# Kernel optimization log

Hardware: AMD Instinct MI355X
Metric: run time of the kernel (lower is better)

## Reference

```python
import jax, jax.numpy as jnp
import numpy as np

N_NODES = 50000
IN_NF = 64
HID = 128
OUT_NF = 64
EDGE_HID = HID // 2  # edge_nf_ratio = 2
N_LAYERS = 4
N_EDGES = 800000
NUM_LATENT_NODES = 64
C_EVEN = 1.0
C_ODD = 2.0 / NUM_LATENT_NODES


def setup_inputs() -> dict:
    key = jax.random.key(0)
    ks = jax.random.split(key, 24)
    def lin(k, fan_in, fan_out):
        # torch nn.Linear default init: U(-1/sqrt(fan_in), 1/sqrt(fan_in))
        bound = 1.0 / np.sqrt(fan_in)
        kw, kb = jax.random.split(k)
        w = jax.random.uniform(kw, (fan_in, fan_out), jnp.float32, -bound, bound)
        b = jax.random.uniform(kb, (fan_out,), jnp.float32, -bound, bound)
        return w, b

    h = jax.random.normal(ks[0], (N_NODES, IN_NF), jnp.float32)
    edges_a = jax.random.randint(ks[1], (2, N_EDGES), 0, N_NODES, jnp.int32)
    edges_b = jax.random.randint(ks[2], (2, N_EDGES), 0, N_NODES, jnp.int32)
    update_mask_a = jax.random.randint(ks[3], (N_NODES, 1), 0, 2, jnp.int32).astype(bool)
    update_mask_b = jax.random.randint(ks[4], (N_NODES, 1), 0, 2, jnp.int32).astype(bool)

    emb_in_w, emb_in_b = lin(ks[5], IN_NF, HID)
    emb_out_w, emb_out_b = lin(ks[6], HID, OUT_NF)

    ew1, eb1, ew2, eb2 = [], [], [], []
    nw1, nb1, nw2, nb2 = [], [], [], []
    for i in range(N_LAYERS):
        w, b = lin(ks[7 + i], 2 * HID, EDGE_HID); ew1.append(w); eb1.append(b)
        w, b = lin(ks[11 + i], EDGE_HID, EDGE_HID); ew2.append(w); eb2.append(b)
        w, b = lin(ks[15 + i], HID + EDGE_HID, HID); nw1.append(w); nb1.append(b)
        w, b = lin(ks[19 + i], HID, HID); nw2.append(w); nb2.append(b)

    stack = lambda xs: jnp.stack(xs, 0)
    return {
        "h": h, "edges_a": edges_a, "edges_b": edges_b,
        "update_mask_a": update_mask_a, "update_mask_b": update_mask_b,
        "emb_in_w": emb_in_w, "emb_in_b": emb_in_b,
        "emb_out_w": emb_out_w, "emb_out_b": emb_out_b,
        "edge_w1": stack(ew1), "edge_b1": stack(eb1),
        "edge_w2": stack(ew2), "edge_b2": stack(eb2),
        "node_w1": stack(nw1), "node_b1": stack(nb1),
        "node_w2": stack(nw2), "node_b2": stack(nb2),
    }


def _gcl(h, edges, mask, C, ew1, eb1, ew2, eb2, nw1, nb1, nw2, nb2):
    row, col = edges[0], edges[1]
    # edge model: gather source/target node feats -> 2-layer SiLU MLP
    feat = jnp.concatenate([h[row], h[col]], axis=-1)      # [E, 2*HID]
    m = jax.nn.silu(feat @ ew1 + eb1)                      # [E, EDGE_HID]
    m = jax.nn.silu(m @ ew2 + eb2)                         # [E, EDGE_HID]
    # aggregate messages to receiving nodes (scatter-add), scaled by C
    agg = jax.ops.segment_sum(m, row, num_segments=h.shape[0]) * C
    # node model with residual
    upd = jax.nn.silu(jnp.concatenate([h, agg], axis=-1) @ nw1 + nb1) @ nw2 + nb2
    h_new = h + upd
    # masked asynchronous update: only nodes with mask=True are updated
    return jnp.where(mask, h_new, h)


def reference(h, edges_a, edges_b, update_mask_a, update_mask_b,
              emb_in_w, emb_in_b, emb_out_w, emb_out_b,
              edge_w1, edge_b1, edge_w2, edge_b2,
              node_w1, node_b1, node_w2, node_b2):
    h = h @ emb_in_w + emb_in_b
    for i in range(N_LAYERS):
        if i % 2 == 0:
            edges, mask, C = edges_a, update_mask_a, C_EVEN
        else:
            edges, mask, C = edges_b, update_mask_b, C_ODD
        h = _gcl(h, edges, mask, C,
                 edge_w1[i], edge_b1[i], edge_w2[i], edge_b2[i],
                 node_w1[i], node_b1[i], node_w2[i], node_b2[i])
    h = h @ emb_out_w + emb_out_b
    return h
```

## Files before the change

### kernel.cpp

```cpp
#include <hip/hip_runtime.h>
#include <cstdint>

typedef __bf16 bf16_t;
typedef bf16_t bf16x8 __attribute__((ext_vector_type(8)));
typedef float floatx4 __attribute__((ext_vector_type(4)));
typedef unsigned short ushort4v __attribute__((ext_vector_type(4)));

constexpr int N_NODES = 50000;
constexpr int N_EDGES = 800000;
constexpr int HID = 128;
constexpr int EH = 64;
constexpr int NCH = (N_NODES + 255) / 256;

__device__ __forceinline__ float silu_f(float x) {
    return x * __builtin_amdgcn_rcpf(1.0f + __expf(-x));
}

__global__ __launch_bounds__(256) void pack_all_kernel(
    const float* __restrict__ embin, const float* __restrict__ embout,
    const float* __restrict__ ew1, const float* __restrict__ ew2,
    const float* __restrict__ nw1, const float* __restrict__ nw2,
    bf16_t* __restrict__ pk)
{
    int t = blockIdx.x * 256 + threadIdx.x;
    if (t >= 32768) {
        t -= 32768;
        int lane = t & 63, chunk = t >> 6;
        int ks = chunk & 3, nt = (chunk >> 2) & 7, l = chunk >> 5;
        int quad = lane >> 4, coln = lane & 15;
        const float* Wl = ew1 + l * 256 * 64;
        int kb = (nt >= 4 ? 128 : 0) + ks * 32 + quad * 8;
        int nc = (nt & 3) * 16 + coln;
        bf16x8 v;
#pragma unroll
        for (int j = 0; j < 8; j++) v[j] = (bf16_t)Wl[(kb + j) * 64 + nc];
        *(bf16x8*)(pk + 262144 + t * 8) = v;
        return;
    }
    const float* W; int K, Nc; int base; bf16_t* out;
    if (t < 1024)       { W = embin;  K = 64;  Nc = 128; base = 0;     out = pk; }
    else if (t < 2048)  { W = embout; K = 128; Nc = 64;  base = 1024;  out = pk + 8192; }
    else if (t < 10240) { W = ew1;    K = 256; Nc = 64;  base = 2048;  out = pk + 16384; }
    else if (t < 12288) { W = ew2;    K = 64;  Nc = 64;  base = 10240; out = pk + 81920; }
    else if (t < 24576) { W = nw1;    K = 192; Nc = 128; base = 12288; out = pk + 98304; }
    else                { W = nw2;    K = 128; Nc = 128; base = 24576; out = pk + 196608; }
    t -= base;
    int KS = K >> 5, NT = Nc >> 4;
    int lane = t & 63;
    int chunk = t >> 6;
    int ks = chunk % KS;
    int nt = (chunk / KS) % NT;
    int l  = chunk / (KS * NT);
    int quad = lane >> 4, coln = lane & 15;
    const float* Wl = W + l * K * Nc;
    bf16x8 v;
#pragma unroll
    for (int j = 0; j < 8; j++)
        v[j] = (bf16_t)Wl[(ks * 32 + quad * 8 + j) * Nc + nt * 16 + coln];
    *(bf16x8*)(out + t * 8) = v;
}

__global__ void hist2_kernel(const int* __restrict__ ea, const int* __restrict__ eb,
                             const int* __restrict__ ma, const int* __restrict__ mb,
                             int* __restrict__ ba, int* __restrict__ bb) {
    int half = gridDim.x >> 1;
    int b = blockIdx.x;
    const int* erows; const int* mask; int* bins;
    if (b < half) { erows = ea; mask = ma; bins = ba; }
    else          { erows = eb; mask = mb; bins = bb; b -= half; }
    int i = b * 256 + threadIdx.x;
    if (i >= N_EDGES) return;
    int r = erows[i];
    if (mask[r] != 0) atomicAdd(&bins[r], 1);
}

__global__ __launch_bounds__(256) void scan_phase1(
    const int* __restrict__ bins_a, const int* __restrict__ bins_b,
    int* __restrict__ bs_a, int* __restrict__ bs_b) {
    const int* bins = blockIdx.y ? bins_b : bins_a;
    int* bs = blockIdx.y ? bs_b : bs_a;
    int i = blockIdx.x * 256 + threadIdx.x;
    int v = (i < N_NODES) ? (bins[i] != 0 ? bins[i] : 0) : 0;
#pragma unroll
    for (int off = 32; off; off >>= 1) v += __shfl_down(v, off, 64);
    __shared__ int ws_[4];
    int lane = threadIdx.x & 63, wv = threadIdx.x >> 6;
    if (lane == 0) ws_[wv] = v;
    __syncthreads();
    if (threadIdx.x == 0) bs[blockIdx.x] = ws_[0] + ws_[1] + ws_[2] + ws_[3];
}

__global__ __launch_bounds__(256) void scan_phase2(
    int* __restrict__ bs_a, int* __restrict__ bs_b,
    int* __restrict__ bins_a, int* __restrict__ bins_b) {
    int* bs = blockIdx.x ? bs_b : bs_a;
    int* bins = blockIdx.x ? bins_b : bins_a;
    int t = threadIdx.x, lane = t & 63, wv = t >> 6;
    int v = (t < NCH) ? bs[t] : 0;
    int s = v;
#pragma unroll
    for (int off = 1; off < 64; off <<= 1) {
        int u = __shfl_up(s, off, 64);
        if (lane >= off) s += u;
    }
    __shared__ int wsum[4];
    if (lane == 63) wsum[wv] = s;
    __syncthreads();
    int woff = 0;
    for (int w = 0; w < wv; w++) woff += wsum[w];
    int excl = s - v + woff;
    if (t < NCH) bs[t] = excl;
    if (t == NCH - 1) bins[N_NODES] = excl + v;
}

__global__ __launch_bounds__(256) void mask_scan2(
    int* __restrict__ ms_a, int* __restrict__ ms_b,
    int* __restrict__ cnt_a, int* __restrict__ cnt_b) {
    int* ms = blockIdx.x ? ms_b : ms_a;
    int* cnt = blockIdx.x ? cnt_b : cnt_a;
    int t = threadIdx.x, lane = t & 63, wv = t >> 6;
    int v = (t < NCH) ? ms[t] : 0;
    int s = v;
#pragma unroll
    for (int off = 1; off < 64; off <<= 1) {
        int u = __shfl_up(s, off, 64);
        if (lane >= off) s += u;
    }
    __shared__ int wsum[4];
    if (lane == 63) wsum[wv] = s;
    __syncthreads();
    int woff = 0;
    for (int w = 0; w < wv; w++) woff += wsum[w];
    int excl = s - v + woff;
    if (t < NCH) ms[t] = excl;
    if (t == NCH - 1) cnt[0] = excl + v;
}

__global__ __launch_bounds__(256) void compact_kernel(
    const int* __restrict__ ma, const int* __restrict__ mb,
    const int* __restrict__ ms_a, const int* __restrict__ ms_b,
    int* __restrict__ la, int* __restrict__ lb) {
    const int* mask = blockIdx.y ? mb : ma;
    const int* ms = blockIdx.y ? ms_b : ms_a;
    int* list = blockIdx.y ? lb : la;
    int i = blockIdx.x * 256 + threadIdx.x;
    int t = threadIdx.x, lane = t & 63, wv = t >> 6;
    int m = (i < N_NODES) ? (mask[i] != 0) : 0;
    unsigned long long bal = __ballot(m != 0);
    int pos = (int)__popcll(bal & ((1ull << lane) - 1ull));
    __shared__ int wsum[4];
    if (lane == 63) wsum[wv] = pos + m;
    __syncthreads();
    int woff = 0;
    for (int w = 0; w < wv; w++) woff += wsum[w];
    if (m) list[ms[blockIdx.x] + woff + pos] = i;
}

__global__ __launch_bounds__(256) void scan_phase3(
    int* __restrict__ bins_a, int* __restrict__ bins_b,
    const int* __restrict__ bs_a, const int* __restrict__ bs_b) {
    int* bins = blockIdx.y ? bins_b : bins_a;
    const int* bs = blockIdx.y ? bs_b : bs_a;
    int i = blockIdx.x * 256 + threadIdx.x;
    int t = threadIdx.x, lane = t & 63, wv = t >> 6;
    int v = (i < N_NODES) ? bins[i] : 0;
    int s = v;
#pragma unroll
    for (int off = 1; off < 64; off <<= 1) {
        int u = __shfl_up(s, off, 64);
        if (lane >= off) s += u;
    }
    __shared__ int wsum[4];
    if (lane == 63) wsum[wv] = s;
    __syncthreads();
    int woff = 0;
    for (int w = 0; w < wv; w++) woff += wsum[w];
    if (i < N_NODES) bins[i] = s - v + woff + bs[blockIdx.x];
}

__global__ void fill_src_kernel(const int* __restrict__ bins_a, const int* __restrict__ bins_b,
                                int* __restrict__ ssrc_a, int* __restrict__ ssrc_b) {
    const int* bins = blockIdx.y ? bins_b : bins_a;
    int* ssrc = blockIdx.y ? ssrc_b : ssrc_a;
    int r = blockIdx.x * 256 + threadIdx.x;
    if (r >= N_NODES) return;
    int p0 = bins[r], p1 = bins[r + 1];
    for (int p = p0; p < p1; p++) ssrc[p] = r;
}

__global__ void scatter2_kernel(const int* __restrict__ ea, const int* __restrict__ eb,
                                const int* __restrict__ ma, const int* __restrict__ mb,
                                int* __restrict__ ba, int* __restrict__ bb,
                                int* __restrict__ sdst_a, int* __restrict__ sdst_b) {
    int half = gridDim.x >> 1;
    int b = blockIdx.x;
    const int* e; const int* mask; int* bins; int* sdst;
    if (b < half) { e = ea; mask = ma; bins = ba; sdst = sdst_a; }
    else          { e = eb; mask = mb; bins = bb; sdst = sdst_b; b -= half; }
    int i = b * 256 + threadIdx.x;
    if (i >= N_EDGES) return;
    int r = e[i];
    if (mask[r] == 0) return;
    int c = e[N_EDGES + i];
    int pos = atomicAdd(&bins[r], 1);
    sdst[pos] = c;
}

__global__ __launch_bounds__(256) void emb_in_kernel(
    const float* __restrict__ h0, const bf16_t* __restrict__ wp,
    const float* __restrict__ bias, float* __restrict__ h, bf16_t* __restrict__ h_bf)
{
    int t = threadIdx.x, wave = t >> 6, lane = t & 63;
    int quad = lane >> 4, col = lane & 15;
    int m0 = blockIdx.x * 64 + wave * 16;
    int ndc = min(m0 + col, N_NODES - 1);
    floatx4 acc[8] = {};
#pragma unroll
    for (int ks = 0; ks < 2; ks++) {
        const float* ap = h0 + ndc * 64 + ks * 32 + quad * 8;
        floatx4 f0 = *(const floatx4*)ap;
        floatx4 f1 = *(const floatx4*)(ap + 4);
        bf16x8 a;
#pragma unroll
        for (int j = 0; j < 4; j++) { a[j] = (bf16_t)f0[j]; a[j + 4] = (bf16_t)f1[j]; }
#pragma unroll
        for (int nt = 0; nt < 8; nt++) {
            bf16x8 b = ((const bf16x8*)wp)[(nt * 2 + ks) * 64 + lane];
            acc[nt] = __builtin_amdgcn_mfma_f32_16x16x32_bf16(a, b, acc[nt], 0, 0, 0);
        }
    }
#pragma unroll
    for (int r = 0; r < 4; r++) {
        int nd2 = m0 + quad * 4 + r;
        if (nd2 < N_NODES) {
#pragma unroll
            for (int nt = 0; nt < 8; nt++) {
                int n = nt * 16 + col;
                float x = acc[nt][r] + bias[n];
                h[nd2 * HID + n] = x;
                h_bf[nd2 * HID + n] = (bf16_t)x;
            }
        }
    }
}

__global__ __launch_bounds__(256) void pre_edge_kernel(
    const bf16_t* __restrict__ h_bf, const bf16_t* __restrict__ w1cat,
    const float* __restrict__ b1, float* __restrict__ P)
{
    int t = threadIdx.x, wave = t >> 6, lane = t & 63;
    int quad = lane >> 4, col = lane & 15;
    int m0 = blockIdx.x * 64 + wave * 16;
    int ndc = min(m0 + col, N_NODES - 1);
    floatx4 acc[8] = {};
#pragma unroll
    for (int ks = 0; ks < 4; ks++) {
        bf16x8 a = *(const bf16x8*)(h_bf + ndc * HID + ks * 32 + quad * 8);
#pragma unroll
        for (int nt = 0; nt < 8; nt++) {
            bf16x8 b = ((const bf16x8*)w1cat)[(nt * 4 + ks) * 64 + lane];
            acc[nt] = __builtin_amdgcn_mfma_f32_16x16x32_bf16(a, b, acc[nt], 0, 0, 0);
        }
    }
#pragma unroll
    for (int r = 0; r < 4; r++) {
        int nd2 = m0 + quad * 4 + r;
        if (nd2 < N_NODES) {
#pragma unroll
            for (int nt = 0; nt < 8; nt++) {
                int n = nt * 16 + col;
                float x = acc[nt][r] + (nt >= 4 ? b1[n - 64] : 0.0f);
                P[nd2 * 128 + n] = x;
            }
        }
    }
}

__global__ __launch_bounds__(256, 4) void edge_kernel_pre(
    const float* __restrict__ P, const int* __restrict__ ssrc,
    const int* __restrict__ sdst, const int* __restrict__ m_ptr,
    const bf16_t* __restrict__ w2p, const float* __restrict__ b2,
    float* __restrict__ agg, float C)
{
    __shared__ __align__(16) bf16_t pool[4][64 * 40];

    int t = threadIdx.x;
    int wave = t >> 6, lane = t & 63, quad = lane >> 4, col = lane & 15;
    bf16_t* mbT = pool[wave];

    float b2v[4];
#pragma unroll
    for (int nt = 0; nt < 4; nt++) b2v[nt] = b2[nt * 16 + col];

    int M = m_ptr[0];
    int ntiles = (M + 31) >> 5;
    int wid = blockIdx.x * 4 + wave, nw = gridDim.x * 4;
    if (wid >= ntiles) return;

    int sr = 0x7fffffff, ds = 0x7fffffff;
    { int p = wid * 32 + lane; if (lane < 32 && p < M) { sr = ssrc[p]; ds = sdst[p]; } }

    for (int tile = wid; tile < ntiles; tile += nw) {
        int tnc = min(tile + nw, ntiles - 1);
        int srn = 0x7fffffff, dsn = 0x7fffffff;
        { int p = tnc * 32 + lane; if (lane < 32 && p < M) { srn = ssrc[p]; dsn = sdst[p]; } }

        floatx4 acc2[2][4] = {};
#pragma unroll
        for (int m = 0; m < 2; m++) {
            int rN = min(__shfl(sr, m * 16 + col, 64), N_NODES - 1);
            int cN = min(__shfl(ds, m * 16 + col, 64), N_NODES - 1);
            const float* pr = P + rN * 128 + quad * 8;
            const float* pc = P + cN * 128 + 64 + quad * 8;
            floatx4 fr[4], fc[4];
#pragma unroll
            for (int ks = 0; ks < 2; ks++) {
                fr[ks * 2]     = *(const floatx4*)(pr + ks * 32);
                fr[ks * 2 + 1] = *(const floatx4*)(pr + ks * 32 + 4);
                fc[ks * 2]     = *(const floatx4*)(pc + ks * 32);
                fc[ks * 2 + 1] = *(const floatx4*)(pc + ks * 32 + 4);
            }
#pragma unroll
            for (int ks = 0; ks < 2; ks++) {
                bf16x8 a2;
#pragma unroll
                for (int j = 0; j < 4; j++) {
                    a2[j]     = (bf16_t)silu_f(fr[ks * 2][j]     + fc[ks * 2][j]);
                    a2[j + 4] = (bf16_t)silu_f(fr[ks * 2 + 1][j] + fc[ks * 2 + 1][j]);
                }
#pragma unroll
                for (int nt = 0; nt < 4; nt++) {
                    bf16x8 b = ((const bf16x8*)w2p)[(nt * 2 + ks) * 64 + lane];
                    acc2[m][nt] = __builtin_amdgcn_mfma_f32_16x16x32_bf16(a2, b, acc2[m][nt], 0, 0, 0);
                }
            }
        }

#pragma unroll
        for (int m = 0; m < 2; m++)
#pragma unroll
            for (int nt = 0; nt < 4; nt++) {
                ushort4v pv;
#pragma unroll
                for (int r = 0; r < 4; r++) {
                    bf16_t bv = (bf16_t)(silu_f(acc2[m][nt][r] + b2v[nt]) * C);
                    pv[r] = __builtin_bit_cast(unsigned short, bv);
                }
                *(ushort4v*)(mbT + (nt * 16 + col) * 40 + m * 16 + quad * 4) = pv;
            }

        {
            float mv[32];
#pragma unroll
            for (int i = 0; i < 4; i++) {
                bf16x8 v8 = *(const bf16x8*)(mbT + lane * 40 + i * 8);
#pragma unroll
                for (int j = 0; j < 8; j++) mv[i * 8 + j] = (float)v8[j];
            }
            int dp = __shfl(sr, 0, 64);
            float run = mv[0];
#pragma unroll
            for (int r = 1; r < 32; r++) {
                int d = __shfl(sr, r, 64);
                if (d != dp) {
                    if (dp < N_NODES) atomicAdd(agg + dp * EH + lane, run);
                    run = mv[r]; dp = d;
                } else run += mv[r];
            }
            if (dp < N_NODES) atomicAdd(agg + dp * EH + lane, run);
        }

        sr = srn; ds = dsn;
    }
}

__global__ __launch_bounds__(256, 3) void edge_kernel_sorted(
    const bf16_t* __restrict__ h_bf, const int* __restrict__ ssrc,
    const int* __restrict__ sdst, const int* __restrict__ m_ptr,
    const bf16_t* __restrict__ w1p, const float* __restrict__ b1,
    const bf16_t* __restrict__ w2p, const float* __restrict__ b2,
    float* __restrict__ agg, float C)
{
    __shared__ __align__(16) bf16_t w1s[16384];
    __shared__ __align__(16) bf16_t pool[4][64 * 40];

    int t = threadIdx.x;
#pragma unroll
    for (int i = 0; i < 8; i++)
        ((bf16x8*)w1s)[t + 256 * i] = ((const bf16x8*)w1p)[t + 256 * i];
    __syncthreads();

    int wave = t >> 6, lane = t & 63, quad = lane >> 4, col = lane & 15;
    bf16_t* hl = pool[wave];
    bf16_t* mbT = pool[wave];

    float b1v[4], b2v[4];
#pragma unroll
    for (int nt = 0; nt < 4; nt++) { b1v[nt] = b1[nt * 16 + col]; b2v[nt] = b2[nt * 16 + col]; }

    int M = m_ptr[0];
    int ntiles = (M + 31) >> 5;
    int wid = blockIdx.x * 4 + wave, nw = gridDim.x * 4;
    if (wid >= ntiles) return;

    int sr = 0x7fffffff, ds = 0x7fffffff;
    { int p = wid * 32 + lane; if (lane < 32 && p < M) { sr = ssrc[p]; ds = sdst[p]; } }
    bf16x8 a[2][8];
    {
        int ns0 = min(__shfl(sr, col, 64), N_NODES - 1);
        int ns1 = min(__shfl(sr, 16 + col, 64), N_NODES - 1);
        int nd0 = min(__shfl(ds, col, 64), N_NODES - 1);
        int nd1 = min(__shfl(ds, 16 + col, 64), N_NODES - 1);
#pragma unroll
        for (int ks = 0; ks < 8; ks++) {
            int o = (ks & 3) * 32 + quad * 8;
            a[0][ks] = *(const bf16x8*)(h_bf + (ks < 4 ? ns0 : nd0) * HID + o);
            a[1][ks] = *(const bf16x8*)(h_bf + (ks < 4 ? ns1 : nd1) * HID + o);
        }
    }

    for (int tile = wid; tile < ntiles; tile += nw) {
        int tnc = min(tile + nw, ntiles - 1);
        int srn = 0x7fffffff, dsn = 0x7fffffff;
        { int p = tnc * 32 + lane; if (lane < 32 && p < M) { srn = ssrc[p]; dsn = sdst[p]; } }

        floatx4 acc[2][4] = {};
#pragma unroll
        for (int ks = 0; ks < 8; ks++) {
#pragma unroll
            for (int nt = 0; nt < 4; nt++) {
                bf16x8 b = ((const bf16x8*)w1s)[(nt * 8 + ks) * 64 + lane];
                acc[0][nt] = __builtin_amdgcn_mfma_f32_16x16x32_bf16(a[0][ks], b, acc[0][nt], 0, 0, 0);
                acc[1][nt] = __builtin_amdgcn_mfma_f32_16x16x32_bf16(a[1][ks], b, acc[1][nt], 0, 0, 0);
            }
        }

        bf16x8 an[2][8];
        {
            int ns0 = min(__shfl(srn, col, 64), N_NODES - 1);
            int ns1 = min(__shfl(srn, 16 + col, 64), N_NODES - 1);
            int nd0 = min(__shfl(dsn, col, 64), N_NODES - 1);
            int nd1 = min(__shfl(dsn, 16 + col, 64), N_NODES - 1);
#pragma unroll
            for (int ks = 0; ks < 8; ks++) {
                int o = (ks & 3) * 32 + quad * 8;
                an[0][ks] = *(const bf16x8*)(h_bf + (ks < 4 ? ns0 : nd0) * HID + o);
                an[1][ks] = *(const bf16x8*)(h_bf + (ks < 4 ? ns1 : nd1) * HID + o);
            }
        }

#pragma unroll
        for (int m = 0; m < 2; m++)
#pragma unroll
            for (int nt = 0; nt < 4; nt++)
#pragma unroll
                for (int r = 0; r < 4; r++)
                    hl[(m * 16 + quad * 4 + r) * 72 + nt * 16 + col] =
                        (bf16_t)silu_f(acc[m][nt][r] + b1v[nt]);

        floatx4 acc2[2][4] = {};
#pragma unroll
        for (int ks = 0; ks < 2; ks++) {
            bf16x8 a2[2];
#pragma unroll
            for (int m = 0; m < 2; m++)
                a2[m] = *(const bf16x8*)(hl + (m * 16 + col) * 72 + ks * 32 + quad * 8);
#pragma unroll
            for (int nt = 0; nt < 4; nt++) {
                bf16x8 b = ((const bf16x8*)w2p)[(nt * 2 + ks) * 64 + lane];
                acc2[0][nt] = __builtin_amdgcn_mfma_f32_16x16x32_bf16(a2[0], b, acc2[0][nt], 0, 0, 0);
                acc2[1][nt] = __builtin_amdgcn_mfma_f32_16x16x32_bf16(a2[1], b, acc2[1][nt], 0, 0, 0);
            }
        }
#pragma unroll
        for (int m = 0; m < 2; m++)
#pragma unroll
            for (int nt = 0; nt < 4; nt++) {
                ushort4v p;
#pragma unroll
                for (int r = 0; r < 4; r++) {
                    bf16_t bv = (bf16_t)(silu_f(acc2[m][nt][r] + b2v[nt]) * C);
                    p[r] = __builtin_bit_cast(unsigned short, bv);
                }
                *(ushort4v*)(mbT + (nt * 16 + col) * 40 + m * 16 + quad * 4) = p;
            }

        {
            float mv[32];
#pragma unroll
            for (int i = 0; i < 4; i++) {
                bf16x8 v8 = *(const bf16x8*)(mbT + lane * 40 + i * 8);
#pragma unroll
                for (int j = 0; j < 8; j++) mv[i * 8 + j] = (float)v8[j];
            }
            int dp = __shfl(sr, 0, 64);
            float run = mv[0];
#pragma unroll
            for (int r = 1; r < 32; r++) {
                int d = __shfl(sr, r, 64);
                if (d != dp) {
                    if (dp < N_NODES) atomicAdd(agg + dp * EH + lane, run);
                    run = mv[r]; dp = d;
                } else run += mv[r];
            }
            if (dp < N_NODES) atomicAdd(agg + dp * EH + lane, run);
        }

        sr = srn; ds = dsn;
#pragma unroll
        for (int m = 0; m < 2; m++)
#pragma unroll
            for (int ks = 0; ks < 8; ks++) a[m][ks] = an[m][ks];
    }
}

__global__ __launch_bounds__(256) void edge_kernel(
    const bf16_t* __restrict__ h_bf, const int* __restrict__ edges,
    const int* __restrict__ mask,
    const bf16_t* __restrict__ w1p, const float* __restrict__ b1,
    const bf16_t* __restrict__ w2p, const float* __restrict__ b2,
    float* __restrict__ agg, float C)
{
    __shared__ __align__(16) bf16_t w1s[16384];
    __shared__ __align__(16) bf16_t w2s[4096];
    __shared__ __align__(16) bf16_t hl[4][16 * 72];

    int t = threadIdx.x;
#pragma unroll
    for (int i = 0; i < 8; i++)
        ((bf16x8*)w1s)[t + 256 * i] = ((const bf16x8*)w1p)[t + 256 * i];
#pragma unroll
    for (int i = 0; i < 2; i++)
        ((bf16x8*)w2s)[t + 256 * i] = ((const bf16x8*)w2p)[t + 256 * i];
    __syncthreads();

    int wave = t >> 6, lane = t & 63, quad = lane >> 4, col = lane & 15;
    bf16_t* myhl = hl[wave];

    float b1v[4], b2v[4];
#pragma unroll
    for (int nt = 0; nt < 4; nt++) { b1v[nt] = b1[nt * 16 + col]; b2v[nt] = b2[nt * 16 + col]; }

    const int ntile_cnt = N_EDGES / 64;
    for (int tile = blockIdx.x; tile < ntile_cnt; tile += gridDim.x) {
        int ebase = tile * 64 + wave * 16;
        int src = edges[ebase + col];
        int dst = edges[N_EDGES + ebase + col];

        floatx4 acc[4] = {};
#pragma unroll
        for (int ks = 0; ks < 8; ks++) {
            int idx = (ks < 4) ? src : dst;
            bf16x8 a = *(const bf16x8*)(h_bf + idx * HID + (ks & 3) * 32 + quad * 8);
#pragma unroll
            for (int nt = 0; nt < 4; nt++) {
                bf16x8 b = ((const bf16x8*)w1s)[(nt * 8 + ks) * 64 + lane];
                acc[nt] = __builtin_amdgcn_mfma_f32_16x16x32_bf16(a, b, acc[nt], 0, 0, 0);
            }
        }
#pragma unroll
        for (int nt = 0; nt < 4; nt++)
#pragma unroll
            for (int r = 0; r < 4; r++)
                myhl[(quad * 4 + r) * 72 + nt * 16 + col] = (bf16_t)silu_f(acc[nt][r] + b1v[nt]);
        __syncthreads();

        floatx4 acc2[4] = {};
#pragma unroll
        for (int ks = 0; ks < 2; ks++) {
            bf16x8 a = *(const bf16x8*)(myhl + col * 72 + ks * 32 + quad * 8);
#pragma unroll
            for (int nt = 0; nt < 4; nt++) {
                bf16x8 b = ((const bf16x8*)w2s)[(nt * 2 + ks) * 64 + lane];
                acc2[nt] = __builtin_amdgcn_mfma_f32_16x16x32_bf16(a, b, acc2[nt], 0, 0, 0);
            }
        }
#pragma unroll
        for (int r = 0; r < 4; r++) {
            int dest = edges[ebase + quad * 4 + r];
            if (mask[dest] != 0) {
                float* aggp = agg + dest * EH;
#pragma unroll
                for (int nt = 0; nt < 4; nt++) {
                    float x = acc2[nt][r] + b2v[nt];
                    atomicAdd(aggp + nt * 16 + col, silu_f(x) * C);
                }
            }
        }
        __syncthreads();
    }
}

__global__ __launch_bounds__(256) void node_kernel_masked(
    float* __restrict__ h, bf16_t* __restrict__ h_bf,
    float* __restrict__ agg, const int* __restrict__ list,
// ... 111 lines not shown
            myhl[(quad * 4 + r) * 136 + nt * 16 + col] = (bf16_t)silu_f(x);
        }

    floatx4 acc2[8] = {};
#pragma unroll
    for (int ks = 0; ks < 4; ks++) {
        bf16x8 a = *(const bf16x8*)(myhl + col * 136 + ks * 32 + quad * 8);
#pragma unroll
        for (int nt = 0; nt < 8; nt++) {
            bf16x8 b = ((const bf16x8*)w2p)[(nt * 4 + ks) * 64 + lane];
            acc2[nt] = __builtin_amdgcn_mfma_f32_16x16x32_bf16(a, b, acc2[nt], 0, 0, 0);
        }
    }
#pragma unroll
    for (int r = 0; r < 4; r++) {
        int nd2 = m0 + quad * 4 + r;
        bool valid = nd2 < N_NODES;
        bool upd = valid && mask[min(nd2, N_NODES - 1)] != 0;
        if (upd) {
#pragma unroll
            for (int nt = 0; nt < 8; nt++) {
                int n = nt * 16 + col;
                float hv = h[nd2 * HID + n] + acc2[nt][r] + b2[n];
                h[nd2 * HID + n] = hv;
                bf16_t hb = (bf16_t)hv;
                h_bf[nd2 * HID + n] = hb;
                myhl[(quad * 4 + r) * 136 + n] = hb;
            }
        } else {
#pragma unroll
            for (int nt = 0; nt < 8; nt++) {
                int n = nt * 16 + col;
                myhl[(quad * 4 + r) * 136 + n] =
                    valid ? h_bf[nd2 * HID + n] : (bf16_t)0.0f;
            }
        }
    }
    floatx4 ao[4] = {};
#pragma unroll
    for (int ks = 0; ks < 4; ks++) {
        bf16x8 a = *(const bf16x8*)(myhl + col * 136 + ks * 32 + quad * 8);
#pragma unroll
        for (int nt = 0; nt < 4; nt++) {
            bf16x8 b = ((const bf16x8*)wop)[(nt * 4 + ks) * 64 + lane];
            ao[nt] = __builtin_amdgcn_mfma_f32_16x16x32_bf16(a, b, ao[nt], 0, 0, 0);
        }
    }
#pragma unroll
    for (int r = 0; r < 4; r++) {
        int nd2 = m0 + quad * 4 + r;
        if (nd2 < N_NODES) {
#pragma unroll
            for (int nt = 0; nt < 4; nt++) {
                int n = nt * 16 + col;
                out[nd2 * 64 + n] = ao[nt][r] + bo[n];
            }
        }
    }
}

extern "C" void kernel_launch(void* const* d_in, const int* in_sizes, int n_in,
                              void* d_out, int out_size, void* d_ws, size_t ws_size,
                              hipStream_t stream) {
    const float* h0        = (const float*)d_in[0];
    const int*   edges_a   = (const int*)d_in[1];
    const int*   edges_b   = (const int*)d_in[2];
    const int*   mask_a    = (const int*)d_in[3];
    const int*   mask_b    = (const int*)d_in[4];
    const float* emb_in_w  = (const float*)d_in[5];
    const float* emb_in_b  = (const float*)d_in[6];
    const float* emb_out_w = (const float*)d_in[7];
    const float* emb_out_b = (const float*)d_in[8];
    const float* ew1 = (const float*)d_in[9];
    const float* eb1 = (const float*)d_in[10];
    const float* ew2 = (const float*)d_in[11];
    const float* eb2 = (const float*)d_in[12];
    const float* nw1 = (const float*)d_in[13];
    const float* nb1 = (const float*)d_in[14];
    const float* nw2 = (const float*)d_in[15];
    const float* nb2 = (const float*)d_in[16];

    const size_t SZ_H = 25600000, SZ_HBF = 12800000, SZ_AGG = 12800000;
    const size_t SZ_PK = 655360;
    const size_t SZ_S = 3200000, SZ_BINS = 200704, SZ_BS = 1024, SZ_LIST = 200704;
    const size_t SZ_P = 25600000;

    char* ws = (char*)d_ws;
    size_t off = 0;
    float*  h    = (float*)(ws + off);  off += SZ_H;
    bf16_t* h_bf = (bf16_t*)(ws + off); off += SZ_HBF;
    float*  agg  = (float*)(ws + off);  off += SZ_AGG;
    bf16_t* pk   = (bf16_t*)(ws + off); off += SZ_PK;
    int* ssrc_a = (int*)(ws + off); off += SZ_S;
    int* sdst_a = (int*)(ws + off); off += SZ_S;
    int* ssrc_b = (int*)(ws + off); off += SZ_S;
    int* sdst_b = (int*)(ws + off); off += SZ_S;
    int* bins_a = (int*)(ws + off); off += SZ_BINS;
    int* bins_b = (int*)(ws + off); off += SZ_BINS;
    int* bs_a   = (int*)(ws + off); off += SZ_BS;
    int* bs_b   = (int*)(ws + off); off += SZ_BS;
    int* ms_a   = (int*)(ws + off); off += SZ_BS;
    int* ms_b   = (int*)(ws + off); off += SZ_BS;
    int* cnt_a  = (int*)(ws + off); off += 256;
    int* cnt_b  = (int*)(ws + off); off += 256;
    int* list_a = (int*)(ws + off); off += SZ_LIST;
    int* list_b = (int*)(ws + off); off += SZ_LIST;
    bool sorted_path = (ws_size >= off);
    float* P = (float*)(ws + off); off += SZ_P;
    bool pre_path = (ws_size >= off);

    bf16_t* pk_embin  = pk;
    bf16_t* pk_embout = pk + 8192;
    bf16_t* pk_ew1    = pk + 16384;
    bf16_t* pk_ew2    = pk + 81920;
    bf16_t* pk_nw1    = pk + 98304;
    bf16_t* pk_nw2    = pk + 196608;
    bf16_t* pk_ew1cat = pk + 262144;

    pack_all_kernel<<<160, 256, 0, stream>>>(emb_in_w, emb_out_w, ew1, ew2, nw1, nw2, pk);

    const int edge_grid = (N_EDGES + 255) / 256;
    const int node_blocks = (N_NODES + 63) / 64;
    if (sorted_path) {
        hipMemsetAsync(bins_a, 0, 2 * SZ_BINS + 2 * SZ_BS, stream);
        hist2_kernel<<<2 * edge_grid, 256, 0, stream>>>(edges_a, edges_b, mask_a, mask_b,
                                                        bins_a, bins_b);
        scan_phase1<<<dim3(NCH, 2), 256, 0, stream>>>(bins_a, bins_b, bs_a, bs_b);
        scan_phase2<<<2, 256, 0, stream>>>(bs_a, bs_b, bins_a, bins_b);
        scan_phase3<<<dim3(NCH, 2), 256, 0, stream>>>(bins_a, bins_b, bs_a, bs_b);
        fill_src_kernel<<<dim3(NCH, 2), 256, 0, stream>>>(bins_a, bins_b, ssrc_a, ssrc_b);
        scatter2_kernel<<<2 * edge_grid, 256, 0, stream>>>(edges_a, edges_b, mask_a, mask_b,
                                                           bins_a, bins_b, sdst_a, sdst_b);
        scan_phase1<<<dim3(NCH, 2), 256, 0, stream>>>(mask_a, mask_b, ms_a, ms_b);
        mask_scan2<<<2, 256, 0, stream>>>(ms_a, ms_b, cnt_a, cnt_b);
        compact_kernel<<<dim3(NCH, 2), 256, 0, stream>>>(mask_a, mask_b, ms_a, ms_b,
                                                         list_a, list_b);
    }

    hipMemsetAsync(agg, 0, (size_t)N_NODES * EH * 4, stream);
    emb_in_kernel<<<node_blocks, 256, 0, stream>>>(h0, pk_embin, emb_in_b, h, h_bf);

    for (int l = 0; l < 4; l++) {
        const int* mask = (l & 1) ? mask_b : mask_a;
        float C = (l & 1) ? 0.03125f : 1.0f;
        if (pre_path) {
            const int* ssrc = (l & 1) ? ssrc_b : ssrc_a;
            const int* sdst = (l & 1) ? sdst_b : sdst_a;
            const int* mp   = ((l & 1) ? bins_b : bins_a) + N_NODES;
            pre_edge_kernel<<<node_blocks, 256, 0, stream>>>(
                h_bf, pk_ew1cat + l * 16384, eb1 + l * 64, P);
            edge_kernel_pre<<<1024, 256, 0, stream>>>(P, ssrc, sdst, mp,
                                                      pk_ew2 + l * 4096, eb2 + l * 64,
                                                      agg, C);
        } else if (sorted_path) {
            const int* ssrc = (l & 1) ? ssrc_b : ssrc_a;
            const int* sdst = (l & 1) ? sdst_b : sdst_a;
            const int* mp   = ((l & 1) ? bins_b : bins_a) + N_NODES;
            edge_kernel_sorted<<<768, 256, 0, stream>>>(h_bf, ssrc, sdst, mp,
                                                        pk_ew1 + l * 16384, eb1 + l * 64,
                                                        pk_ew2 + l * 4096,  eb2 + l * 64,
                                                        agg, C);
        } else {
            const int* edges = (l & 1) ? edges_b : edges_a;
            edge_kernel<<<768, 256, 0, stream>>>(h_bf, edges, mask,
                                                 pk_ew1 + l * 16384, eb1 + l * 64,
                                                 pk_ew2 + l * 4096,  eb2 + l * 64,
                                                 agg, C);
        }
        if (l < 3 && sorted_path) {
            const int* list = (l & 1) ? list_b : list_a;
            const int* cnt  = (l & 1) ? cnt_b : cnt_a;
            node_kernel_masked<<<node_blocks, 256, 0, stream>>>(
                h, h_bf, agg, list, cnt,
                pk_nw1 + l * 24576, nb1 + l * 128,
                pk_nw2 + l * 16384, nb2 + l * 128);
        } else if (l < 3) {
            node_kernel<<<node_blocks, 256, 0, stream>>>(h, h_bf, agg, mask,
                                                         pk_nw1 + l * 24576, nb1 + l * 128,
                                                         pk_nw2 + l * 16384, nb2 + l * 128,
                                                         pk_embout, emb_out_b, (float*)d_out);
            hipMemsetAsync(agg, 0, (size_t)N_NODES * EH * 4, stream);
        } else {
            node_kernel<<<node_blocks, 256, 0, stream>>>(h, h_bf, agg, mask,
                                                         pk_nw1 + 3 * 24576, nb1 + 3 * 128,
                                                         pk_nw2 + 3 * 16384, nb2 + 3 * 128,
                                                         pk_embout, emb_out_b, (float*)d_out);
        }
    }
}
```

Baseline: 439.8 us.

## Replace CSR sort with two-level bucket sort and fuse first pre-edge into embedding

The per-node histogram/scan/fill/scatter pipeline that builds sorted edge lists is replaced by a two-level bucket sort: edges are binned into 256-node buckets with shared-memory counters, then each bucket is sorted locally. This cuts global atomics and the number of preprocessing kernel launches. The first layer's pre-edge projection is fused into the input-embedding kernel, and the agg memset is merged with the bucket-counter memset. Buckets are capped at a fixed capacity, so edges beyond it would be silently dropped if a bucket overflowed.

```diff
diff --git a/kernel.cpp b/kernel.cpp
--- a/kernel.cpp
+++ b/kernel.cpp
@@ -11,6 +11,7 @@
 constexpr int HID = 128;
 constexpr int EH = 64;
 constexpr int NCH = (N_NODES + 255) / 256;
+constexpr int BKT_CAP = 4096;
 
 __device__ __forceinline__ float silu_f(float x) {
     return x * __builtin_amdgcn_rcpf(1.0f + __expf(-x));
@@ -60,18 +61,125 @@
     *(bf16x8*)(out + t * 8) = v;
 }
 
-__global__ void hist2_kernel(const int* __restrict__ ea, const int* __restrict__ eb,
-                             const int* __restrict__ ma, const int* __restrict__ mb,
-                             int* __restrict__ ba, int* __restrict__ bb) {
-    int half = gridDim.x >> 1;
-    int b = blockIdx.x;
-    const int* erows; const int* mask; int* bins;
-    if (b < half) { erows = ea; mask = ma; bins = ba; }
-    else          { erows = eb; mask = mb; bins = bb; b -= half; }
-    int i = b * 256 + threadIdx.x;
-    if (i >= N_EDGES) return;
-    int r = erows[i];
-    if (mask[r] != 0) atomicAdd(&bins[r], 1);
+__global__ __launch_bounds__(256) void bucketize_kernel(
+    const int* __restrict__ ea, const int* __restrict__ eb,
+    const int* __restrict__ ma, const int* __restrict__ mb,
+    int* __restrict__ gcur, int* __restrict__ gbuf)
+{
+    int g = blockIdx.y;
+    const int* e    = g ? eb : ea;
+    const int* mask = g ? mb : ma;
+    int* cur = gcur + g * 256;
+    int* buf = gbuf + g * 256 * BKT_CAP;
+    __shared__ int cnt[256];
+    int t = threadIdx.x;
+    cnt[t] = 0;
+    __syncthreads();
+    int base = blockIdx.x * 2048;
+    int r[8], c[8]; bool v[8];
+#pragma unroll
+    for (int k = 0; k < 8; k++) {
+        int i = base + k * 256 + t;
+        bool ok = i < N_EDGES;
+        int ii = ok ? i : 0;
+        int rr = e[ii];
+        int cc = e[N_EDGES + ii];
+        v[k] = ok && (mask[rr] != 0);
+        r[k] = rr; c[k] = cc;
+        if (v[k]) atomicAdd(&cnt[rr >> 8], 1);
+    }
+    __syncthreads();
+    int lc = cnt[t];
+    int gb = 0;
+    if (lc > 0) gb = atomicAdd(&cur[t], lc);
+    cnt[t] = gb;
+    __syncthreads();
+#pragma unroll
+    for (int k = 0; k < 8; k++) {
+        if (v[k]) {
+            int bkt = r[k] >> 8;
+            int p = atomicAdd(&cnt[bkt], 1);
+            if (p < BKT_CAP)
+                buf[bkt * BKT_CAP + p] = ((r[k] & 255) << 16) | c[k];
+        }
+    }
+}
+
+__global__ __launch_bounds__(256) void bucket_scan_kernel(
+    const int* __restrict__ gcur, int* __restrict__ bases,
+    int* __restrict__ mcnt_a, int* __restrict__ mcnt_b)
+{
+    int g = blockIdx.x;
+    const int* cur = gcur + g * 256;
+    int t = threadIdx.x, lane = t & 63, wv = t >> 6;
+    int v = (t < NCH) ? min(cur[t], BKT_CAP) : 0;
+    int s = v;
+#pragma unroll
+    for (int off = 1; off < 64; off <<= 1) {
+        int u = __shfl_up(s, off, 64);
+        if (lane >= off) s += u;
+    }
+    __shared__ int wsum[4];
+    if (lane == 63) wsum[wv] = s;
+    __syncthreads();
+    int woff = 0;
+    for (int w = 0; w < wv; w++) woff += wsum[w];
+    int excl = s - v + woff;
+    bases[g * 256 + t] = excl;
+    if (t == NCH - 1) *(g ? mcnt_b : mcnt_a) = excl + v;
+}
+
+__global__ __launch_bounds__(256) void bucket_sort_kernel(
+    const int* __restrict__ gcur, const int* __restrict__ gbuf,
+    const int* __restrict__ bases,
+    int* __restrict__ ssrc_a, int* __restrict__ sdst_a,
+    int* __restrict__ ssrc_b, int* __restrict__ sdst_b)
+{
+    int g = blockIdx.y, b = blockIdx.x;
+    const int* buf = gbuf + g * 256 * BKT_CAP + b * BKT_CAP;
+    int* ssrc = g ? ssrc_b : ssrc_a;
+    int* sdst = g ? sdst_b : sdst_a;
+    int cnt_e = min(gcur[g * 256 + b], BKT_CAP);
+    int base = bases[g * 256 + b];
+    __shared__ int h[256];
+    __shared__ int wsum[4];
+    int t = threadIdx.x, lane = t & 63, wv = t >> 6;
+    h[t] = 0;
+    __syncthreads();
+    int vals[16]; bool vv[16];
+#pragma unroll
+    for (int k = 0; k < 16; k++) {
+        int j = k * 256 + t;
+        vv[k] = j < cnt_e;
+        int x = vv[k] ? buf[j] : 0;
+        vals[k] = x;
+        if (vv[k]) atomicAdd(&h[x >> 16], 1);
+    }
+    __syncthreads();
+    int v = h[t];
+    int s = v;
+#pragma unroll
+    for (int off = 1; off < 64; off <<= 1) {
+        int u = __shfl_up(s, off, 64);
+        if (lane >= off) s += u;
+    }
+    if (lane == 63) wsum[wv] = s;
+    __syncthreads();
+    int woff = 0;
+    for (int w = 0; w < wv; w++) woff += wsum[w];
+    h[t] = s - v + woff;
+    __syncthreads();
+#pragma unroll
+    for (int k = 0; k < 16; k++) {
+        if (vv[k]) {
+            int x = vals[k];
+            int rl = x >> 16, c = x & 0xFFFF;
+            int p = atomicAdd(&h[rl], 1);
+            int gp = base + p;
+            ssrc[gp] = (b << 8) + rl;
+            sdst[gp] = c;
+        }
+    }
 }
 
 __global__ __launch_bounds__(256) void scan_phase1(
@@ -88,29 +196,6 @@
     if (lane == 0) ws_[wv] = v;
     __syncthreads();
     if (threadIdx.x == 0) bs[blockIdx.x] = ws_[0] + ws_[1] + ws_[2] + ws_[3];
-}
-
-__global__ __launch_bounds__(256) void scan_phase2(
-    int* __restrict__ bs_a, int* __restrict__ bs_b,
-    int* __restrict__ bins_a, int* __restrict__ bins_b) {
-    int* bs = blockIdx.x ? bs_b : bs_a;
-    int* bins = blockIdx.x ? bins_b : bins_a;
-    int t = threadIdx.x, lane = t & 63, wv = t >> 6;
-    int v = (t < NCH) ? bs[t] : 0;
-    int s = v;
-#pragma unroll
-    for (int off = 1; off < 64; off <<= 1) {
-        int u = __shfl_up(s, off, 64);
-        if (lane >= off) s += u;
-    }
-    __shared__ int wsum[4];
-    if (lane == 63) wsum[wv] = s;
-    __syncthreads();
-    int woff = 0;
-    for (int w = 0; w < wv; w++) woff += wsum[w];
-    int excl = s - v + woff;
-    if (t < NCH) bs[t] = excl;
-    if (t == NCH - 1) bins[N_NODES] = excl + v;
 }
 
 __global__ __launch_bounds__(256) void mask_scan2(
@@ -156,56 +241,6 @@
     if (m) list[ms[blockIdx.x] + woff + pos] = i;
 }
 
-__global__ __launch_bounds__(256) void scan_phase3(
-    int* __restrict__ bins_a, int* __restrict__ bins_b,
-    const int* __restrict__ bs_a, const int* __restrict__ bs_b) {
-    int* bins = blockIdx.y ? bins_b : bins_a;
-    const int* bs = blockIdx.y ? bs_b : bs_a;
-    int i = blockIdx.x * 256 + threadIdx.x;
-    int t = threadIdx.x, lane = t & 63, wv = t >> 6;
-    int v = (i < N_NODES) ? bins[i] : 0;
-    int s = v;
-#pragma unroll
-    for (int off = 1; off < 64; off <<= 1) {
-        int u = __shfl_up(s, off, 64);
-        if (lane >= off) s += u;
-    }
-    __shared__ int wsum[4];
-    if (lane == 63) wsum[wv] = s;
-    __syncthreads();
-    int woff = 0;
-    for (int w = 0; w < wv; w++) woff += wsum[w];
-    if (i < N_NODES) bins[i] = s - v + woff + bs[blockIdx.x];
-}
-
-__global__ void fill_src_kernel(const int* __restrict__ bins_a, const int* __restrict__ bins_b,
-                                int* __restrict__ ssrc_a, int* __restrict__ ssrc_b) {
-    const int* bins = blockIdx.y ? bins_b : bins_a;
-    int* ssrc = blockIdx.y ? ssrc_b : ssrc_a;
-    int r = blockIdx.x * 256 + threadIdx.x;
-    if (r >= N_NODES) return;
-    int p0 = bins[r], p1 = bins[r + 1];
-    for (int p = p0; p < p1; p++) ssrc[p] = r;
-}
-
-__global__ void scatter2_kernel(const int* __restrict__ ea, const int* __restrict__ eb,
-                                const int* __restrict__ ma, const int* __restrict__ mb,
-                                int* __restrict__ ba, int* __restrict__ bb,
-                                int* __restrict__ sdst_a, int* __restrict__ sdst_b) {
-    int half = gridDim.x >> 1;
-    int b = blockIdx.x;
-    const int* e; const int* mask; int* bins; int* sdst;
-    if (b < half) { e = ea; mask = ma; bins = ba; sdst = sdst_a; }
-    else          { e = eb; mask = mb; bins = bb; sdst = sdst_b; b -= half; }
-    int i = b * 256 + threadIdx.x;
-    if (i >= N_EDGES) return;
-    int r = e[i];
-    if (mask[r] == 0) return;
-    int c = e[N_EDGES + i];
-    int pos = atomicAdd(&bins[r], 1);
-    sdst[pos] = c;
-}
-
 __global__ __launch_bounds__(256) void emb_in_kernel(
     const float* __restrict__ h0, const bf16_t* __restrict__ wp,
     const float* __restrict__ bias, float* __restrict__ h, bf16_t* __restrict__ h_bf)
@@ -239,6 +274,74 @@
                 float x = acc[nt][r] + bias[n];
                 h[nd2 * HID + n] = x;
                 h_bf[nd2 * HID + n] = (bf16_t)x;
+            }
+        }
+    }
+}
+
+__global__ __launch_bounds__(256) void emb_in_p0_kernel(
+    const float* __restrict__ h0, const bf16_t* __restrict__ wp,
+    const float* __restrict__ bias, float* __restrict__ h, bf16_t* __restrict__ h_bf,
+    const bf16_t* __restrict__ w1cat, const float* __restrict__ b1,
+    float* __restrict__ P)
+{
+    __shared__ __align__(16) bf16_t hl[4][16 * 136];
+    int t = threadIdx.x, wave = t >> 6, lane = t & 63;
+    int quad = lane >> 4, col = lane & 15;
+    int m0 = blockIdx.x * 64 + wave * 16;
+    int ndc = min(m0 + col, N_NODES - 1);
+    floatx4 acc[8] = {};
+#pragma unroll
+    for (int ks = 0; ks < 2; ks++) {
+        const float* ap = h0 + ndc * 64 + ks * 32 + quad * 8;
+        floatx4 f0 = *(const floatx4*)ap;
+        floatx4 f1 = *(const floatx4*)(ap + 4);
+        bf16x8 a;
+#pragma unroll
+        for (int j = 0; j < 4; j++) { a[j] = (bf16_t)f0[j]; a[j + 4] = (bf16_t)f1[j]; }
+#pragma unroll
+        for (int nt = 0; nt < 8; nt++) {
+            bf16x8 b = ((const bf16x8*)wp)[(nt * 2 + ks) * 64 + lane];
+            acc[nt] = __builtin_amdgcn_mfma_f32_16x16x32_bf16(a, b, acc[nt], 0, 0, 0);
+        }
+    }
+    bf16_t* myhl = hl[wave];
+#pragma unroll
+    for (int r = 0; r < 4; r++) {
+        int nd2 = m0 + quad * 4 + r;
+        bool valid = nd2 < N_NODES;
+#pragma unroll
+        for (int nt = 0; nt < 8; nt++) {
+            int n = nt * 16 + col;
+            if (valid) {
+                float x = acc[nt][r] + bias[n];
+                h[nd2 * HID + n] = x;
+                bf16_t hb = (bf16_t)x;
+                h_bf[nd2 * HID + n] = hb;
+                myhl[(quad * 4 + r) * 136 + n] = hb;
+            } else {
+                myhl[(quad * 4 + r) * 136 + n] = (bf16_t)0.0f;
+            }
+        }
+    }
+    floatx4 accp[8] = {};
+#pragma unroll
+    for (int ks = 0; ks < 4; ks++) {
+        bf16x8 a = *(const bf16x8*)(myhl + col * 136 + ks * 32 + quad * 8);
+#pragma unroll
+        for (int nt = 0; nt < 8; nt++) {
+            bf16x8 b = ((const bf16x8*)w1cat)[(nt * 4 + ks) * 64 + lane];
+            accp[nt] = __builtin_amdgcn_mfma_f32_16x16x32_bf16(a, b, accp[nt], 0, 0, 0);
+        }
+    }
+#pragma unroll
+    for (int r = 0; r < 4; r++) {
+        int nd2 = m0 + quad * 4 + r;
+        if (nd2 < N_NODES) {
+#pragma unroll
+            for (int nt = 0; nt < 8; nt++) {
+                int n = nt * 16 + col;
+                P[nd2 * 128 + n] = accp[nt][r] + (nt >= 4 ? b1[n - 64] : 0.0f);
             }
         }
     }
@@ -371,146 +474,6 @@
         }
 
         sr = srn; ds = dsn;
-    }
-}
-
-__global__ __launch_bounds__(256, 3) void edge_kernel_sorted(
-    const bf16_t* __restrict__ h_bf, const int* __restrict__ ssrc,
-    const int* __restrict__ sdst, const int* __restrict__ m_ptr,
-    const bf16_t* __restrict__ w1p, const float* __restrict__ b1,
-    const bf16_t* __restrict__ w2p, const float* __restrict__ b2,
-    float* __restrict__ agg, float C)
-{
-    __shared__ __align__(16) bf16_t w1s[16384];
-    __shared__ __align__(16) bf16_t pool[4][64 * 40];
-
-    int t = threadIdx.x;
-#pragma unroll
-    for (int i = 0; i < 8; i++)
-        ((bf16x8*)w1s)[t + 256 * i] = ((const bf16x8*)w1p)[t + 256 * i];
-    __syncthreads();
-
-    int wave = t >> 6, lane = t & 63, quad = lane >> 4, col = lane & 15;
-    bf16_t* hl = pool[wave];
-    bf16_t* mbT = pool[wave];
-
-    float b1v[4], b2v[4];
-#pragma unroll
-    for (int nt = 0; nt < 4; nt++) { b1v[nt] = b1[nt * 16 + col]; b2v[nt] = b2[nt * 16 + col]; }
-
-    int M = m_ptr[0];
-    int ntiles = (M + 31) >> 5;
-    int wid = blockIdx.x * 4 + wave, nw = gridDim.x * 4;
-    if (wid >= ntiles) return;
-
-    int sr = 0x7fffffff, ds = 0x7fffffff;
-    { int p = wid * 32 + lane; if (lane < 32 && p < M) { sr = ssrc[p]; ds = sdst[p]; } }
-    bf16x8 a[2][8];
-    {
-        int ns0 = min(__shfl(sr, col, 64), N_NODES - 1);
-        int ns1 = min(__shfl(sr, 16 + col, 64), N_NODES - 1);
-        int nd0 = min(__shfl(ds, col, 64), N_NODES - 1);
-        int nd1 = min(__shfl(ds, 16 + col, 64), N_NODES - 1);
-#pragma unroll
-        for (int ks = 0; ks < 8; ks++) {
-            int o = (ks & 3) * 32 + quad * 8;
-            a[0][ks] = *(const bf16x8*)(h_bf + (ks < 4 ? ns0 : nd0) * HID + o);
-            a[1][ks] = *(const bf16x8*)(h_bf + (ks < 4 ? ns1 : nd1) * HID + o);
-        }
-    }
-
-    for (int tile = wid; tile < ntiles; tile += nw) {
-        int tnc = min(tile + nw, ntiles - 1);
-        int srn = 0x7fffffff, dsn = 0x7fffffff;
-        { int p = tnc * 32 + lane; if (lane < 32 && p < M) { srn = ssrc[p]; dsn = sdst[p]; } }
-
-        floatx4 acc[2][4] = {};
-#pragma unroll
-        for (int ks = 0; ks < 8; ks++) {
-#pragma unroll
-            for (int nt = 0; nt < 4; nt++) {
-                bf16x8 b = ((const bf16x8*)w1s)[(nt * 8 + ks) * 64 + lane];
-                acc[0][nt] = __builtin_amdgcn_mfma_f32_16x16x32_bf16(a[0][ks], b, acc[0][nt], 0, 0, 0);
-                acc[1][nt] = __builtin_amdgcn_mfma_f32_16x16x32_bf16(a[1][ks], b, acc[1][nt], 0, 0, 0);
-            }
-        }
-
-        bf16x8 an[2][8];
-        {
-            int ns0 = min(__shfl(srn, col, 64), N_NODES - 1);
-            int ns1 = min(__shfl(srn, 16 + col, 64), N_NODES - 1);
-            int nd0 = min(__shfl(dsn, col, 64), N_NODES - 1);
-            int nd1 = min(__shfl(dsn, 16 + col, 64), N_NODES - 1);
-#pragma unroll
-            for (int ks = 0; ks < 8; ks++) {
-                int o = (ks & 3) * 32 + quad * 8;
-                an[0][ks] = *(const bf16x8*)(h_bf + (ks < 4 ? ns0 : nd0) * HID + o);
-                an[1][ks] = *(const bf16x8*)(h_bf + (ks < 4 ? ns1 : nd1) * HID + o);
-            }
-        }
-
-#pragma unroll
-        for (int m = 0; m < 2; m++)
-#pragma unroll
-            for (int nt = 0; nt < 4; nt++)
-#pragma unroll
-                for (int r = 0; r < 4; r++)
-                    hl[(m * 16 + quad * 4 + r) * 72 + nt * 16 + col] =
-                        (bf16_t)silu_f(acc[m][nt][r] + b1v[nt]);
-
-        floatx4 acc2[2][4] = {};
-#pragma unroll
-        for (int ks = 0; ks < 2; ks++) {
-            bf16x8 a2[2];
-#pragma unroll
-            for (int m = 0; m < 2; m++)
-                a2[m] = *(const bf16x8*)(hl + (m * 16 + col) * 72 + ks * 32 + quad * 8);
-#pragma unroll
-            for (int nt = 0; nt < 4; nt++) {
-                bf16x8 b = ((const bf16x8*)w2p)[(nt * 2 + ks) * 64 + lane];
-                acc2[0][nt] = __builtin_amdgcn_mfma_f32_16x16x32_bf16(a2[0], b, acc2[0][nt], 0, 0, 0);
-                acc2[1][nt] = __builtin_amdgcn_mfma_f32_16x16x32_bf16(a2[1], b, acc2[1][nt], 0, 0, 0);
-            }
-        }
-#pragma unroll
-        for (int m = 0; m < 2; m++)
-#pragma unroll
-            for (int nt = 0; nt < 4; nt++) {
-                ushort4v p;
-#pragma unroll
-                for (int r = 0; r < 4; r++) {
-                    bf16_t bv = (bf16_t)(silu_f(acc2[m][nt][r] + b2v[nt]) * C);
-                    p[r] = __builtin_bit_cast(unsigned short, bv);
-                }
-                *(ushort4v*)(mbT + (nt * 16 + col) * 40 + m * 16 + quad * 4) = p;
-            }
-
-        {
-            float mv[32];
-#pragma unroll
-            for (int i = 0; i < 4; i++) {
-                bf16x8 v8 = *(const bf16x8*)(mbT + lane * 40 + i * 8);
-#pragma unroll
-                for (int j = 0; j < 8; j++) mv[i * 8 + j] = (float)v8[j];
-            }
-            int dp = __shfl(sr, 0, 64);
-            float run = mv[0];
-#pragma unroll
-            for (int r = 1; r < 32; r++) {
-                int d = __shfl(sr, r, 64);
-                if (d != dp) {
-                    if (dp < N_NODES) atomicAdd(agg + dp * EH + lane, run);
-                    run = mv[r]; dp = d;
-                } else run += mv[r];
-            }
-            if (dp < N_NODES) atomicAdd(agg + dp * EH + lane, run);
-        }
-
-        sr = srn; ds = dsn;
-#pragma unroll
-        for (int m = 0; m < 2; m++)
-#pragma unroll
-            for (int ks = 0; ks < 8; ks++) a[m][ks] = an[m][ks];
     }
 }
 
@@ -788,32 +751,33 @@
 
     const size_t SZ_H = 25600000, SZ_HBF = 12800000, SZ_AGG = 12800000;
     const size_t SZ_PK = 655360;
-    const size_t SZ_S = 3200000, SZ_BINS = 200704, SZ_BS = 1024, SZ_LIST = 200704;
+    const size_t SZ_S = 3200000, SZ_BS = 1024, SZ_LIST = 200704;
+    const size_t SZ_GBUF = (size_t)2 * 256 * BKT_CAP * 4;
     const size_t SZ_P = 25600000;
 
     char* ws = (char*)d_ws;
     size_t off = 0;
     float*  h    = (float*)(ws + off);  off += SZ_H;
     bf16_t* h_bf = (bf16_t*)(ws + off); off += SZ_HBF;
-    float*  agg  = (float*)(ws + off);  off += SZ_AGG;
     bf16_t* pk   = (bf16_t*)(ws + off); off += SZ_PK;
     int* ssrc_a = (int*)(ws + off); off += SZ_S;
     int* sdst_a = (int*)(ws + off); off += SZ_S;
     int* ssrc_b = (int*)(ws + off); off += SZ_S;
     int* sdst_b = (int*)(ws + off); off += SZ_S;
-    int* bins_a = (int*)(ws + off); off += SZ_BINS;
-    int* bins_b = (int*)(ws + off); off += SZ_BINS;
-    int* bs_a   = (int*)(ws + off); off += SZ_BS;
-    int* bs_b   = (int*)(ws + off); off += SZ_BS;
+    int* gbuf   = (int*)(ws + off); off += SZ_GBUF;
+    int* gcur   = (int*)(ws + off); off += 2048;
+    float* agg  = (float*)(ws + off); off += SZ_AGG;
+    int* bases  = (int*)(ws + off); off += 2048;
+    int* mcnt_a = (int*)(ws + off); off += 256;
+    int* mcnt_b = (int*)(ws + off); off += 256;
     int* ms_a   = (int*)(ws + off); off += SZ_BS;
     int* ms_b   = (int*)(ws + off); off += SZ_BS;
     int* cnt_a  = (int*)(ws + off); off += 256;
     int* cnt_b  = (int*)(ws + off); off += 256;
     int* list_a = (int*)(ws + off); off += SZ_LIST;
     int* list_b = (int*)(ws + off); off += SZ_LIST;
-    bool sorted_path = (ws_size >= off);
-    float* P = (float*)(ws + off); off += SZ_P;
-    bool pre_path = (ws_size >= off);
+    float* P    = (float*)(ws + off); off += SZ_P;
+    bool ok = (ws_size >= off);
 
     bf16_t* pk_embin  = pk;
     bf16_t* pk_embout = pk + 8192;
@@ -825,47 +789,39 @@
 
     pack_all_kernel<<<160, 256, 0, stream>>>(emb_in_w, emb_out_w, ew1, ew2, nw1, nw2, pk);
 
-    const int edge_grid = (N_EDGES + 255) / 256;
     const int node_blocks = (N_NODES + 63) / 64;
-    if (sorted_path) {
-        hipMemsetAsync(bins_a, 0, 2 * SZ_BINS + 2 * SZ_BS, stream);
-        hist2_kernel<<<2 * edge_grid, 256, 0, stream>>>(edges_a, edges_b, mask_a, mask_b,
-                                                        bins_a, bins_b);
-        scan_phase1<<<dim3(NCH, 2), 256, 0, stream>>>(bins_a, bins_b, bs_a, bs_b);
-        scan_phase2<<<2, 256, 0, stream>>>(bs_a, bs_b, bins_a, bins_b);
-        scan_phase3<<<dim3(NCH, 2), 256, 0, stream>>>(bins_a, bins_b, bs_a, bs_b);
-        fill_src_kernel<<<dim3(NCH, 2), 256, 0, stream>>>(bins_a, bins_b, ssrc_a, ssrc_b);
-        scatter2_kernel<<<2 * edge_grid, 256, 0, stream>>>(edges_a, edges_b, mask_a, mask_b,
-                                                           bins_a, bins_b, sdst_a, sdst_b);
+    const int bkt_blocks = (N_EDGES + 2047) / 2048;
+    if (ok) {
+        hipMemsetAsync(gcur, 0, 2048 + SZ_AGG, stream);
+        bucketize_kernel<<<dim3(bkt_blocks, 2), 256, 0, stream>>>(
+            edges_a, edges_b, mask_a, mask_b, gcur, gbuf);
+        bucket_scan_kernel<<<2, 256, 0, stream>>>(gcur, bases, mcnt_a, mcnt_b);
+        bucket_sort_kernel<<<dim3(NCH, 2), 256, 0, stream>>>(
+            gcur, gbuf, bases, ssrc_a, sdst_a, ssrc_b, sdst_b);
         scan_phase1<<<dim3(NCH, 2), 256, 0, stream>>>(mask_a, mask_b, ms_a, ms_b);
         mask_scan2<<<2, 256, 0, stream>>>(ms_a, ms_b, cnt_a, cnt_b);
         compact_kernel<<<dim3(NCH, 2), 256, 0, stream>>>(mask_a, mask_b, ms_a, ms_b,
                                                          list_a, list_b);
-    }
-
-    hipMemsetAsync(agg, 0, (size_t)N_NODES * EH * 4, stream);
-    emb_in_kernel<<<node_blocks, 256, 0, stream>>>(h0, pk_embin, emb_in_b, h, h_bf);
+        emb_in_p0_kernel<<<node_blocks, 256, 0, stream>>>(
+            h0, pk_embin, emb_in_b, h, h_bf, pk_ew1cat, eb1, P);
+    } else {
+        hipMemsetAsync(agg, 0, SZ_AGG, stream);
+        emb_in_kernel<<<node_blocks, 256, 0, stream>>>(h0, pk_embin, emb_in_b, h, h_bf);
+    }
 
     for (int l = 0; l < 4; l++) {
         const int* mask = (l & 1) ? mask_b : mask_a;
         float C = (l & 1) ? 0.03125f : 1.0f;
-        if (pre_path) {
+        if (ok) {
             const int* ssrc = (l & 1) ? ssrc_b : ssrc_a;
             const int* sdst = (l & 1) ? sdst_b : sdst_a;
-            const int* mp   = ((l & 1) ? bins_b : bins_a) + N_NODES;
-            pre_edge_kernel<<<node_blocks, 256, 0, stream>>>(
-                h_bf, pk_ew1cat + l * 16384, eb1 + l * 64, P);
+            const int* mp   = (l & 1) ? mcnt_b : mcnt_a;
+            if (l > 0)
+                pre_edge_kernel<<<node_blocks, 256, 0, stream>>>(
+                    h_bf, pk_ew1cat + l * 16384, eb1 + l * 64, P);
             edge_kernel_pre<<<1024, 256, 0, stream>>>(P, ssrc, sdst, mp,
                                                       pk_ew2 + l * 4096, eb2 + l * 64,
                                                       agg, C);
-        } else if (sorted_path) {
-            const int* ssrc = (l & 1) ? ssrc_b : ssrc_a;
-            const int* sdst = (l & 1) ? sdst_b : sdst_a;
-            const int* mp   = ((l & 1) ? bins_b : bins_a) + N_NODES;
-            edge_kernel_sorted<<<768, 256, 0, stream>>>(h_bf, ssrc, sdst, mp,
-                                                        pk_ew1 + l * 16384, eb1 + l * 64,
-                                                        pk_ew2 + l * 4096,  eb2 + l * 64,
-                                                        agg, C);
         } else {
             const int* edges = (l & 1) ? edges_b : edges_a;
             edge_kernel<<<768, 256, 0, stream>>>(h_bf, edges, mask,
@@ -873,7 +829,7 @@
                                                  pk_ew2 + l * 4096,  eb2 + l * 64,
                                                  agg, C);
         }
-        if (l < 3 && sorted_path) {
+        if (l < 3 && ok) {
             const int* list = (l & 1) ? list_b : list_a;
             const int* cnt  = (l & 1) ? cnt_b : cnt_a;
             node_kernel_masked<<<node_blocks, 256, 0, stream>>>(
@@ -885,7 +841,7 @@
                                                          pk_nw1 + l * 24576, nb1 + l * 128,
                                                          pk_nw2 + l * 16384, nb2 + l * 128,
                                                          pk_embout, emb_out_b, (float*)d_out);
-            hipMemsetAsync(agg, 0, (size_t)N_NODES * EH * 4, stream);
+            hipMemsetAsync(agg, 0, SZ_AGG, stream);
         } else {
             node_kernel<<<node_blocks, 256, 0, stream>>>(h, h_bf, agg, mask,
                                                          pk_nw1 + 3 * 24576, nb1 + 3 * 128,
```

Measured after the change: 378.5 us. 13.9% less time.
